# Performance work log

Measured on AMD Instinct MI355X. Metric: run time of the kernel, lower is better.

## Reference

```python
import jax, jax.numpy as jnp
import numpy as np


def setup_inputs() -> dict:
    key = jax.random.key(0)
    k1, k2, k3 = jax.random.split(key, 3)
    N, RANK, M = 1024, 16, 4096
    W = jax.random.normal(k1, (N, RANK), dtype=jnp.float32)
    H = jax.random.normal(k2, (RANK, M), dtype=jnp.float32)
    tau_tilde = jax.random.uniform(k3, (N, RANK), dtype=jnp.float32)
    return {"W": W, "H": H, "tau_tilde": tau_tilde}


def reference(W, H, tau_tilde):
    # W: (N, rank), H: (rank, M), tau_tilde: (N, rank)
    M = H.shape[1]
    Nf = M // 2 + 1
    # FFT of softplus(H), keep non-negative freqs, rebuild full spectrum by conjugate symmetry
    Hf = jnp.fft.fft(jax.nn.softplus(H), axis=1)[:, :Nf]            # (rank, Nf) complex
    Hf_reverse = Hf[:, 1:Nf - 1][:, ::-1]                            # flip of interior bins
    Hft = jnp.concatenate([Hf, jnp.conj(Hf_reverse)], axis=1)        # (rank, M)
    f = jnp.arange(M, dtype=jnp.float32) / M                         # (M,)
    # omega[N,d,M] = exp(-i 2 pi tau[N,d] f[M]); Wf = softplus(W)[...,None] * omega
    omega = jnp.exp(-2j * jnp.pi * (tau_tilde[:, :, None] * f[None, None, :]))
    Wf = jax.nn.softplus(W)[:, :, None].astype(omega.dtype) * omega  # (N, rank, M)
    V = jnp.einsum('NdM,dM->NM', Wf, Hft)                            # (N, M) complex
    return V
```

## Files before the change

### kernel.cpp

```cpp
#include <hip/hip_runtime.h>
#include <math.h>

#define MLEN 4096
#define RANK 16
#define NROWS 1024
#define LNB 4

__device__ float2 g_Hft[RANK * MLEN];

__device__ __forceinline__ float softplus_f(float x) {
    return fmaxf(x, 0.0f) + log1pf(__expf(-fabsf(x)));
}

#define MAP(i) ((i) + ((i) >> 4))

__global__ __launch_bounds__(1024) void fft_rows_kernel(const float* __restrict__ H) {
    __shared__ float2 buf[MLEN + MLEN / 16];
    const int row = blockIdx.x;
    const int t   = threadIdx.x;
    const float* h = H + row * MLEN;

    const int r10 = (int)(__brev((unsigned)t) >> 22);
    const float a0 = softplus_f(h[r10]);
    const float a1 = softplus_f(h[r10 + 2048]);
    const float a2 = softplus_f(h[r10 + 1024]);
    const float a3 = softplus_f(h[r10 + 3072]);
    const float u0 = a0 + a1, u1 = a0 - a1;
    const float u2 = a2 + a3, u3 = a2 - a3;
    const int k0 = t << 2;
    buf[MAP(k0)]     = make_float2(u0 + u2, 0.0f);
    buf[MAP(k0 + 1)] = make_float2(u1, -u3);
    buf[MAP(k0 + 2)] = make_float2(u0 - u2, 0.0f);
    buf[MAP(k0 + 3)] = make_float2(u1, u3);
    __syncthreads();

    #pragma unroll
    for (int s = 2; s < 12; s += 2) {
        const int h1 = 1 << s;
        const int p  = t & (h1 - 1);
        const int k  = ((t >> s) << (s + 2)) + p;
        const float rA = (float)p * (1.0f / (float)(h1 << 2));
        const float ca = __builtin_amdgcn_cosf(rA);
        const float sa = __builtin_amdgcn_sinf(rA);
        const float c1 = ca * ca - sa * sa;
        const float s1 = 2.0f * ca * sa;

        const float2 a0c = buf[MAP(k)];
        const float2 a1c = buf[MAP(k + h1)];
        const float2 a2c = buf[MAP(k + 2 * h1)];
        const float2 a3c = buf[MAP(k + 3 * h1)];

        const float2 w1a1 = make_float2(c1 * a1c.x + s1 * a1c.y, c1 * a1c.y - s1 * a1c.x);
        const float2 w1a3 = make_float2(c1 * a3c.x + s1 * a3c.y, c1 * a3c.y - s1 * a3c.x);
        const float2 v0 = make_float2(a0c.x + w1a1.x, a0c.y + w1a1.y);
        const float2 v1 = make_float2(a0c.x - w1a1.x, a0c.y - w1a1.y);
        const float2 v2 = make_float2(a2c.x + w1a3.x, a2c.y + w1a3.y);
        const float2 v3 = make_float2(a2c.x - w1a3.x, a2c.y - w1a3.y);

        const float2 wAv2 = make_float2(ca * v2.x + sa * v2.y, ca * v2.y - sa * v2.x);
        const float2 w    = make_float2(ca * v3.x + sa * v3.y, ca * v3.y - sa * v3.x);
        const float2 wBv3 = make_float2(w.y, -w.x);

        buf[MAP(k)]          = make_float2(v0.x + wAv2.x, v0.y + wAv2.y);
        buf[MAP(k + h1)]     = make_float2(v1.x + wBv3.x, v1.y + wBv3.y);
        buf[MAP(k + 2 * h1)] = make_float2(v0.x - wAv2.x, v0.y - wAv2.y);
        buf[MAP(k + 3 * h1)] = make_float2(v1.x - wBv3.x, v1.y - wBv3.y);
        __syncthreads();
    }

    for (int i = t; i < MLEN; i += 1024) {
        g_Hft[row * MLEN + i] = buf[MAP(i)];
    }
}

__global__ __launch_bounds__(256, 6) void mix_mirror_kernel(const float* __restrict__ W,
                                                            const float* __restrict__ tau,
                                                            float* __restrict__ out) {
    __shared__ __align__(16) float4 prm[LNB * RANK];

    const int tid = threadIdx.x;
    const int n0  = blockIdx.y * LNB;

    if (tid < LNB * RANK) {
        const float sw = softplus_f(W[n0 * RANK + tid]);
        const float tv = tau[n0 * RANK + tid];
        const float c2 = __builtin_amdgcn_cosf(tv);
        const float s2 = __builtin_amdgcn_sinf(tv);
        prm[tid] = make_float4(sw, tv, sw * c2, -sw * s2);
    }
    __syncthreads();

    const int a  = blockIdx.x * 256 + tid + 1;
    const int mm = MLEN - a;
    const float fa = (float)a * (1.0f / (float)MLEN);

    float2 h[RANK];
    #pragma unroll
    for (int d = 0; d < RANK; ++d) h[d] = g_Hft[d * MLEN + a];

    #pragma unroll 1
    for (int ln = 0; ln < LNB; ++ln) {
        float ar = 0.0f, aw = 0.0f;
        #pragma unroll
        for (int d = 0; d < RANK; ++d) {
            const float4 P = prm[ln * RANK + d];
            const float r  = P.y * fa;
            const float c  = __builtin_amdgcn_cosf(r);
            const float s  = __builtin_amdgcn_sinf(r);
            const float tre = fmaf(s, h[d].y, c * h[d].x);
            const float tim = fmaf(c, h[d].y, -s * h[d].x);
            ar = fmaf(P.x, tre, ar);
            aw = fmaf(P.z, tre, fmaf(P.w, tim, aw));
        }
        const int rowbase = (n0 + ln) * MLEN;
        out[rowbase + a]  = ar;
        out[rowbase + mm] = aw;
    }

    if (blockIdx.x == 0 && tid == 0) {
        float h0[RANK];
        #pragma unroll
        for (int d = 0; d < RANK; ++d) h0[d] = g_Hft[d * MLEN].x;
        for (int ln = 0; ln < LNB; ++ln) {
            float v = 0.0f;
            #pragma unroll
            for (int d = 0; d < RANK; ++d) v = fmaf(prm[ln * RANK + d].x, h0[d], v);
            out[(n0 + ln) * MLEN] = v;
        }
    }
}

__global__ __launch_bounds__(256) void mix_generic_kernel(const float* __restrict__ W,
                                                          const float* __restrict__ tau,
                                                          float* __restrict__ out,
                                                          int out_size_floats) {
    __shared__ float sw_s[256];
    __shared__ float tau_s[256];
    const int tid = threadIdx.x;
    const int m   = blockIdx.x * 256 + tid;
    const int n0  = blockIdx.y * 16;
    sw_s[tid]  = softplus_f(W[n0 * RANK + tid]);
    tau_s[tid] = tau[n0 * RANK + tid];
    __syncthreads();
    float2 h[RANK];
    #pragma unroll
    for (int d = 0; d < RANK; ++d) h[d] = g_Hft[d * MLEN + m];
    const float fm = (float)m * (1.0f / (float)MLEN);
    #pragma unroll 1
    for (int ln = 0; ln < 16; ++ln) {
        float ar = 0.0f, ai = 0.0f;
        #pragma unroll
        for (int d = 0; d < RANK; ++d) {
            const float r = tau_s[ln * RANK + d] * fm;
            const float c = __builtin_amdgcn_cosf(r);
            const float s = __builtin_amdgcn_sinf(r);
            const float sw = sw_s[ln * RANK + d];
            ar = fmaf(sw, fmaf(s, h[d].y, c * h[d].x), ar);
            ai = fmaf(sw, fmaf(c, h[d].y, -s * h[d].x), ai);
        }
        const long long fi = 2LL * ((long long)(n0 + ln) * MLEN + m);
        if (fi + 1 < (long long)out_size_floats) {
            out[fi]     = ar;
            out[fi + 1] = ai;
        }
    }
}

extern "C" void kernel_launch(void* const* d_in, const int* in_sizes, int n_in,
                              void* d_out, int out_size, void* d_ws, size_t ws_size,
                              hipStream_t stream) {
    const float* W   = (const float*)d_in[0];
    const float* H   = (const float*)d_in[1];
    const float* tau = (const float*)d_in[2];
    float* out = (float*)d_out;
    (void)d_ws; (void)ws_size; (void)in_sizes; (void)n_in;

    fft_rows_kernel<<<dim3(RANK), dim3(1024), 0, stream>>>(H);

    if (out_size == NROWS * MLEN) {
        mix_mirror_kernel<<<dim3(8, NROWS / LNB), dim3(256), 0, stream>>>(W, tau, out);
    } else {
        mix_generic_kernel<<<dim3(MLEN / 256, NROWS / 16), dim3(256), 0, stream>>>(
            W, tau, out, out_size);
    }
}
```

Before: 81.29 us.

## Process two frequency bins per thread using angle-addition twiddle and stage H via LDS

Each thread in the mirror mix kernel now handles bins a and a+1024, deriving the second bin's phase rotation from the first by complex multiplication with a precomputed per-(n,d) rotation exp(-i*tau/4). This halves the sin/cos transcendental evaluations per output and halves the grid in x, at the cost of more registers (occupancy hint lowered from 6 to 4). The FFT kernel also loads its input row with coalesced float4 reads into shared memory instead of bit-reversed scattered global loads. Accuracy of the rotated phase relies on fp32 products rather than direct evaluation.

```diff
diff --git a/kernel.cpp b/kernel.cpp
--- a/kernel.cpp
+++ b/kernel.cpp
@@ -13,6 +13,7 @@
 }
 
 #define MAP(i) ((i) + ((i) >> 4))
+#define SMAP(i) ((i) + ((i) >> 4))
 
 __global__ __launch_bounds__(1024) void fft_rows_kernel(const float* __restrict__ H) {
     __shared__ float2 buf[MLEN + MLEN / 16];
@@ -20,11 +21,21 @@
     const int t   = threadIdx.x;
     const float* h = H + row * MLEN;
 
+    float* sf = (float*)buf;
+    const float4 x4 = reinterpret_cast<const float4*>(h)[t];
+    const int i0 = t << 2;
+    sf[SMAP(i0)]     = x4.x;
+    sf[SMAP(i0 + 1)] = x4.y;
+    sf[SMAP(i0 + 2)] = x4.z;
+    sf[SMAP(i0 + 3)] = x4.w;
+    __syncthreads();
+
     const int r10 = (int)(__brev((unsigned)t) >> 22);
-    const float a0 = softplus_f(h[r10]);
-    const float a1 = softplus_f(h[r10 + 2048]);
-    const float a2 = softplus_f(h[r10 + 1024]);
-    const float a3 = softplus_f(h[r10 + 3072]);
+    const float a0 = softplus_f(sf[SMAP(r10)]);
+    const float a1 = softplus_f(sf[SMAP(r10 + 2048)]);
+    const float a2 = softplus_f(sf[SMAP(r10 + 1024)]);
+    const float a3 = softplus_f(sf[SMAP(r10 + 3072)]);
+    __syncthreads();
     const float u0 = a0 + a1, u1 = a0 - a1;
     const float u2 = a2 + a3, u3 = a2 - a3;
     const int k0 = t << 2;
@@ -73,10 +84,11 @@
     }
 }
 
-__global__ __launch_bounds__(256, 6) void mix_mirror_kernel(const float* __restrict__ W,
+__global__ __launch_bounds__(256, 4) void mix_mirror_kernel(const float* __restrict__ W,
                                                             const float* __restrict__ tau,
                                                             float* __restrict__ out) {
-    __shared__ __align__(16) float4 prm[LNB * RANK];
+    __shared__ __align__(16) float4 prm4[LNB * RANK];
+    __shared__ __align__(16) float2 prm2[LNB * RANK];
 
     const int tid = threadIdx.x;
     const int n0  = blockIdx.y * LNB;
@@ -86,45 +98,61 @@
         const float tv = tau[n0 * RANK + tid];
         const float c2 = __builtin_amdgcn_cosf(tv);
         const float s2 = __builtin_amdgcn_sinf(tv);
-        prm[tid] = make_float4(sw, tv, sw * c2, -sw * s2);
+        const float rc = __builtin_amdgcn_cosf(0.25f * tv);
+        const float rs = __builtin_amdgcn_sinf(0.25f * tv);
+        prm4[tid] = make_float4(sw, tv, sw * c2, -sw * s2);
+        prm2[tid] = make_float2(rc, rs);
     }
     __syncthreads();
 
     const int a  = blockIdx.x * 256 + tid + 1;
-    const int mm = MLEN - a;
+    const int b  = a + 1024;
     const float fa = (float)a * (1.0f / (float)MLEN);
 
-    float2 h[RANK];
+    float2 h0[RANK], h1[RANK];
     #pragma unroll
-    for (int d = 0; d < RANK; ++d) h[d] = g_Hft[d * MLEN + a];
+    for (int d = 0; d < RANK; ++d) {
+        h0[d] = g_Hft[d * MLEN + a];
+        h1[d] = g_Hft[d * MLEN + b];
+    }
 
     #pragma unroll 1
     for (int ln = 0; ln < LNB; ++ln) {
-        float ar = 0.0f, aw = 0.0f;
+        float ar0 = 0.0f, aw0 = 0.0f;
+        float ar1 = 0.0f, aw1 = 0.0f;
         #pragma unroll
         for (int d = 0; d < RANK; ++d) {
-            const float4 P = prm[ln * RANK + d];
+            const float4 P = prm4[ln * RANK + d];
+            const float2 R = prm2[ln * RANK + d];
             const float r  = P.y * fa;
             const float c  = __builtin_amdgcn_cosf(r);
             const float s  = __builtin_amdgcn_sinf(r);
-            const float tre = fmaf(s, h[d].y, c * h[d].x);
-            const float tim = fmaf(c, h[d].y, -s * h[d].x);
-            ar = fmaf(P.x, tre, ar);
-            aw = fmaf(P.z, tre, fmaf(P.w, tim, aw));
+            const float tre0 = fmaf(s, h0[d].y, c * h0[d].x);
+            const float tim0 = fmaf(c, h0[d].y, -s * h0[d].x);
+            ar0 = fmaf(P.x, tre0, ar0);
+            aw0 = fmaf(P.z, tre0, fmaf(P.w, tim0, aw0));
+            const float cb = fmaf(c, R.x, -s * R.y);
+            const float sb = fmaf(s, R.x,  c * R.y);
+            const float tre1 = fmaf(sb, h1[d].y, cb * h1[d].x);
+            const float tim1 = fmaf(cb, h1[d].y, -sb * h1[d].x);
+            ar1 = fmaf(P.x, tre1, ar1);
+            aw1 = fmaf(P.z, tre1, fmaf(P.w, tim1, aw1));
         }
         const int rowbase = (n0 + ln) * MLEN;
-        out[rowbase + a]  = ar;
-        out[rowbase + mm] = aw;
+        out[rowbase + a]          = ar0;
+        out[rowbase + MLEN - a]   = aw0;
+        out[rowbase + b]          = ar1;
+        out[rowbase + MLEN - b]   = aw1;
     }
 
     if (blockIdx.x == 0 && tid == 0) {
-        float h0[RANK];
+        float hdc[RANK];
         #pragma unroll
-        for (int d = 0; d < RANK; ++d) h0[d] = g_Hft[d * MLEN].x;
+        for (int d = 0; d < RANK; ++d) hdc[d] = g_Hft[d * MLEN].x;
         for (int ln = 0; ln < LNB; ++ln) {
             float v = 0.0f;
             #pragma unroll
-            for (int d = 0; d < RANK; ++d) v = fmaf(prm[ln * RANK + d].x, h0[d], v);
+            for (int d = 0; d < RANK; ++d) v = fmaf(prm4[ln * RANK + d].x, hdc[d], v);
             out[(n0 + ln) * MLEN] = v;
         }
     }
@@ -178,7 +206,7 @@
     fft_rows_kernel<<<dim3(RANK), dim3(1024), 0, stream>>>(H);
 
     if (out_size == NROWS * MLEN) {
-        mix_mirror_kernel<<<dim3(8, NROWS / LNB), dim3(256), 0, stream>>>(W, tau, out);
+        mix_mirror_kernel<<<dim3(4, NROWS / LNB), dim3(256), 0, stream>>>(W, tau, out);
     } else {
         mix_generic_kernel<<<dim3(MLEN / 256, NROWS / 16), dim3(256), 0, stream>>>(
             W, tau, out, out_size);
```

After: 81.02 us. No clear change (-0.3%).
